# Kernel tuning notes

Measured on AMD Instinct MI355X. Metric: run time of the kernel, lower is better.

Reference implementation:

```python
import jax, jax.numpy as jnp
import numpy as np
from jax import lax

LEAKY_ALPHA = 0.3  # Keras LeakyReLU default


def _conv2d_same(psi, w, b):
    # psi: [B,H,W,Cin], w: [kh,kw,Cin,Cout], b: [Cout]
    y = lax.conv_general_dilated(
        psi, w, window_strides=(1, 1), padding='SAME',
        dimension_numbers=('NHWC', 'HWIO', 'NHWC'))
    y = y + b
    return jnp.where(y > 0, y, LEAKY_ALPHA * y)


def setup_inputs() -> dict:
    key = jax.random.key(0)
    ks = jax.random.split(key, 4)
    B, H, W, BANDS, C = 2, 128, 128, 32, 64
    CPSI = 64
    x = jax.random.normal(ks[0], (B, H, W, BANDS, C), dtype=jnp.float32)
    psi = jax.random.normal(ks[1], (B, H, W, CPSI), dtype=jnp.float32)
    fan_in = 3 * 3 * CPSI
    scale = (2.0 / fan_in) ** 0.5  # he-like init for conv weights
    gamma_w = jax.random.normal(ks[2], (3, 3, CPSI, C), dtype=jnp.float32) * scale
    beta_w = jax.random.normal(ks[3], (3, 3, CPSI, C), dtype=jnp.float32) * scale
    gamma_b = jnp.zeros((C,), dtype=jnp.float32)
    beta_b = jnp.zeros((C,), dtype=jnp.float32)
    return {"x": x, "psi": psi, "gamma_w": gamma_w, "gamma_b": gamma_b,
            "beta_w": beta_w, "beta_b": beta_b}


def reference(x, psi, gamma_w, gamma_b, beta_w, beta_b):
    # SFT / FiLM: gamma, beta conditioned on psi, broadcast over the band axis.
    gamma = _conv2d_same(psi, gamma_w, gamma_b)  # [B,H,W,C]
    beta = _conv2d_same(psi, beta_w, beta_b)     # [B,H,W,C]
    # Original loops over bands with slice/concat; equivalent to one broadcast.
    return gamma[:, :, :, None, :] * x + beta[:, :, :, None, :]  # [B,H,W,bands,C]
```

## Files before the change

### kernel.cpp

```cpp
#include <hip/hip_runtime.h>


#define LEAKY 0.3f

constexpr int Bc    = 2;
constexpr int Hc    = 128;
constexpr int Wc    = 128;
constexpr int BANDS = 32;
constexpr int C     = 64;
constexpr int CPSI  = 64;
constexpr int COUT2 = 128;
constexpr int NPIX  = Bc * Hc * Wc;

typedef __attribute__((ext_vector_type(8))) short bf16x8;
typedef __attribute__((ext_vector_type(4))) float f32x4;

__device__ __forceinline__ unsigned short f2bf(float v) {
  unsigned int u = __float_as_uint(v);
  u += 0x7fffu + ((u >> 16) & 1u);
  return (unsigned short)(u >> 16);
}
__device__ __forceinline__ float bf2f(unsigned short h) {
  return __uint_as_float(((unsigned int)h) << 16);
}

__global__ __launch_bounds__(256) void split_w(
    const float* __restrict__ gw, const float* __restrict__ bw,
    unsigned short* __restrict__ wt)
{
  int o = blockIdx.x * 256 + threadIdx.x;
  int tap = o >> 14;
  int kp  = (o >> 7) & 127;
  int n   = o & 127;
  int cin = kp & 63;
  const float* src = (n < C) ? gw : bw;
  float v = src[((size_t)tap * 64 + cin) * 64 + (n & 63)];
  unsigned short hi = f2bf(v);
  unsigned short r  = (kp < 64) ? hi : f2bf(v - bf2f(hi));
  wt[((size_t)tap << 14) + (size_t)n * 128 + kp] = r;
}

constexpr int AS_BYTES = 3 * 34 * 136 * 2;
constexpr int BS_BYTES = 128 * 136 * 2;
constexpr int SMEM_BYTES = AS_BYTES + BS_BYTES;

__global__ __launch_bounds__(256) void sft_fused(
    const float* __restrict__ psi,
    const unsigned short* __restrict__ wt,
    const float* __restrict__ gbias, const float* __restrict__ bbias,
    const float* __restrict__ x,
    float* __restrict__ out)
{
  __shared__ __align__(16) char smem[SMEM_BYTES];
  auto As = (unsigned short(*)[34][136])smem;
  auto Bs = (unsigned short(*)[136])(smem + AS_BYTES);
  auto g  = (float(*)[132])smem;

  const int tid = threadIdx.x;
  const int blk = blockIdx.x;
  const int w0  = (blk & 3) * 32;
  const int h   = (blk >> 2) & 127;
  const int b   = blk >> 9;
  const int pix0 = blk * 32;

  for (int c = tid; c < 3 * 34 * 16; c += 256) {
    int ch  = c & 15;
    int col = (c >> 4) % 34;
    int row = (c >> 4) / 34;
    int hh = h + row - 1;
    int ww = w0 + col - 1;
    float4 v = make_float4(0.f, 0.f, 0.f, 0.f);
    if (hh >= 0 && hh < Hc && ww >= 0 && ww < Wc)
      v = *(const float4*)&psi[(((size_t)b * Hc + hh) * Wc + ww) * CPSI + ch * 4];
    ushort4 hi, lo;
    hi.x = f2bf(v.x); lo.x = f2bf(v.x - bf2f(hi.x));
    hi.y = f2bf(v.y); lo.y = f2bf(v.y - bf2f(hi.y));
    hi.z = f2bf(v.z); lo.z = f2bf(v.z - bf2f(hi.z));
    hi.w = f2bf(v.w); lo.w = f2bf(v.w - bf2f(hi.w));
    *(ushort4*)&As[row][col][ch * 4]      = hi;
    *(ushort4*)&As[row][col][64 + ch * 4] = lo;
  }

  const int lane = tid & 63;
  const int wv   = tid >> 6;
  const int nb   = wv * 32;
  const int lrow = lane & 15;
  const int lk8  = (lane >> 4) * 8;

  f32x4 acc[2][2];
#pragma unroll
  for (int i = 0; i < 2; ++i)
#pragma unroll
    for (int j = 0; j < 2; ++j) acc[i][j] = (f32x4){0.f, 0.f, 0.f, 0.f};

  for (int c = tid; c < 128 * 16; c += 256) {
    int ch = c & 15, n = c >> 4;
    *(int4*)&Bs[n][ch * 8] = *(const int4*)&wt[(size_t)n * 128 + ch * 8];
  }
  __syncthreads();

  for (int tap = 0; tap < 9; ++tap) {
    const int r  = tap / 3;
    const int dc = tap % 3;

    int4 wreg[8];
    if (tap < 8) {
      const unsigned short* wsrc = wt + ((size_t)(tap + 1) << 14);
#pragma unroll
      for (int i = 0; i < 8; ++i) {
        int c = tid + 256 * i;
        int ch = c & 15, n = c >> 4;
        wreg[i] = *(const int4*)&wsrc[(size_t)n * 128 + ch * 8];
      }
    }

#pragma unroll
    for (int sb = 0; sb < 3; ++sb) {
      const int ao = (sb == 1) ? 64 : 0;
      const int bo = (sb == 2) ? 64 : 0;
#pragma unroll
      for (int kk = 0; kk < 64; kk += 32) {
        bf16x8 af0 = *(const bf16x8*)&As[r][lrow + dc][ao + kk + lk8];
        bf16x8 af1 = *(const bf16x8*)&As[r][16 + lrow + dc][ao + kk + lk8];
        bf16x8 bf0 = *(const bf16x8*)&Bs[nb + lrow][bo + kk + lk8];
        bf16x8 bf1 = *(const bf16x8*)&Bs[nb + 16 + lrow][bo + kk + lk8];
        acc[0][0] = __builtin_amdgcn_mfma_f32_16x16x32_bf16(af0, bf0, acc[0][0], 0, 0, 0);
        acc[0][1] = __builtin_amdgcn_mfma_f32_16x16x32_bf16(af0, bf1, acc[0][1], 0, 0, 0);
        acc[1][0] = __builtin_amdgcn_mfma_f32_16x16x32_bf16(af1, bf0, acc[1][0], 0, 0, 0);
        acc[1][1] = __builtin_amdgcn_mfma_f32_16x16x32_bf16(af1, bf1, acc[1][1], 0, 0, 0);
      }
    }

    if (tap < 8) {
      __syncthreads();
#pragma unroll
      for (int i = 0; i < 8; ++i) {
        int c = tid + 256 * i;
        int ch = c & 15, n = c >> 4;
        *(int4*)&Bs[n][ch * 8] = wreg[i];
      }
      __syncthreads();
    }
  }

  __syncthreads();
#pragma unroll
  for (int nf = 0; nf < 2; ++nf) {
    const int n = nb + nf * 16 + lrow;
    const float bias = (n < C) ? gbias[n] : bbias[n - C];
#pragma unroll
    for (int mf = 0; mf < 2; ++mf) {
#pragma unroll
      for (int rr = 0; rr < 4; ++rr) {
        int m = mf * 16 + (lane >> 4) * 4 + rr;
        float v = acc[mf][nf][rr] + bias;
        g[m][n] = v > 0.f ? v : LEAKY * v;
      }
    }
  }
  __syncthreads();

  const int c0 = (tid * 4) & 63;
  const size_t pbase = (size_t)pix0 * 2048 + (size_t)tid * 4;
#pragma unroll 4
  for (int p = 0; p < 32; ++p) {
    f32x4 ga = *(const f32x4*)&g[p][c0];
    f32x4 be = *(const f32x4*)&g[p][64 + c0];
    size_t a = pbase + (size_t)p * 2048;
    f32x4 x0 = __builtin_nontemporal_load((const f32x4*)&x[a]);
    f32x4 x1 = __builtin_nontemporal_load((const f32x4*)&x[a + 1024]);
    f32x4 o0, o1;
#pragma unroll
    for (int e = 0; e < 4; ++e) {
      o0[e] = fmaf(ga[e], x0[e], be[e]);
      o1[e] = fmaf(ga[e], x1[e], be[e]);
    }
    __builtin_nontemporal_store(o0, (f32x4*)&out[a]);
    __builtin_nontemporal_store(o1, (f32x4*)&out[a + 1024]);
  }
}

__global__ __launch_bounds__(256) void film_fused_slow(
    const float* __restrict__ psi,
    const float* __restrict__ gw, const float* __restrict__ gbias,
    const float* __restrict__ bw, const float* __restrict__ bbias,
    const float* __restrict__ x,
    float* __restrict__ out)
{
  const int pix = blockIdx.x;
  const int w = pix % Wc;
  const int h = (pix / Wc) % Hc;
  const int b = pix / (Wc * Hc);
  __shared__ float pshal[9 * CPSI];
  __shared__ float g[COUT2];
  const int t = threadIdx.x;

  if (t < 144) {
    int j = t * 4;
    int k = j % CPSI;
    int tap = j / CPSI;
    int r = tap / 3, s = tap % 3;
    int hh = h + r - 1, ww = w + s - 1;
    float4 v = make_float4(0.f, 0.f, 0.f, 0.f);
    if (hh >= 0 && hh < Hc && ww >= 0 && ww < Wc)
      v = *(const float4*)&psi[(((size_t)b * Hc + hh) * Wc + ww) * CPSI + k];
    *(float4*)&pshal[j] = v;
  }
  __syncthreads();

  if (t < COUT2) {
    int c = t & 63;
    const float* W_ = (t < C) ? gw : bw;
    float acc = (t < C) ? gbias[c] : bbias[c];
#pragma unroll 4
    for (int j = 0; j < 576; ++j) acc = fmaf(pshal[j], W_[(size_t)j * 64 + c], acc);
    g[t] = acc > 0.f ? acc : LEAKY * acc;
  }
  __syncthreads();

  const int coff = (t & 7) * 8;
  const size_t base = (size_t)pix * (BANDS * C) + (size_t)t * 8;
  float4 x0 = *(const float4*)&x[base];
  float4 x1 = *(const float4*)&x[base + 4];
  float4 ga0 = *(const float4*)&g[coff];
  float4 ga1 = *(const float4*)&g[coff + 4];
  float4 be0 = *(const float4*)&g[C + coff];
  float4 be1 = *(const float4*)&g[C + coff + 4];
  float4 o0, o1;
  o0.x = fmaf(ga0.x, x0.x, be0.x);
  o0.y = fmaf(ga0.y, x0.y, be0.y);
  o0.z = fmaf(ga0.z, x0.z, be0.z);
  o0.w = fmaf(ga0.w, x0.w, be0.w);
  o1.x = fmaf(ga1.x, x1.x, be1.x);
  o1.y = fmaf(ga1.y, x1.y, be1.y);
  o1.z = fmaf(ga1.z, x1.z, be1.z);
  o1.w = fmaf(ga1.w, x1.w, be1.w);
  *(float4*)&out[base] = o0;
  *(float4*)&out[base + 4] = o1;
}

extern "C" void kernel_launch(void* const* d_in, const int* in_sizes, int n_in,
                              void* d_out, int out_size, void* d_ws, size_t ws_size,
                              hipStream_t stream) {
  const float* x     = (const float*)d_in[0];
  const float* psi   = (const float*)d_in[1];
  const float* gw    = (const float*)d_in[2];
  const float* gbias = (const float*)d_in[3];
  const float* bw    = (const float*)d_in[4];
  const float* bbias = (const float*)d_in[5];
  float* out = (float*)d_out;

  const size_t wsplit_bytes = (size_t)9 * 128 * 128 * 2;

  if (ws_size >= wsplit_bytes) {
    unsigned short* wtp = (unsigned short*)d_ws;
    split_w<<<9 * 128 * 128 / 256, 256, 0, stream>>>(gw, bw, wtp);
    sft_fused<<<NPIX / 32, 256, 0, stream>>>(psi, wtp, gbias, bbias, x, out);
  } else {
    film_fused_slow<<<NPIX, 256, 0, stream>>>(psi, gw, gbias, bw, bbias, x, out);
  }
}
```

Measured before the change: 503.6 us.

## Load MFMA weight fragments directly from global memory instead of LDS staging

Drops the shared-memory weight tile and its per-tap register prefetch plus the two barriers per tap. Each lane now reads its B fragments straight from the global (L2-resident) split weights. This roughly halves LDS use, and the launch bounds now request 4 blocks per CU to raise occupancy. The cost is more global load traffic and latency inside the MFMA loop, with no explicit prefetch to hide it.

After: 464.7 us. 7.7% less time.

```diff
diff --git a/kernel.cpp b/kernel.cpp
--- a/kernel.cpp
+++ b/kernel.cpp
@@ -40,11 +40,9 @@
   wt[((size_t)tap << 14) + (size_t)n * 128 + kp] = r;
 }
 
-constexpr int AS_BYTES = 3 * 34 * 136 * 2;
-constexpr int BS_BYTES = 128 * 136 * 2;
-constexpr int SMEM_BYTES = AS_BYTES + BS_BYTES;
-
-__global__ __launch_bounds__(256) void sft_fused(
+constexpr int SMEM_BYTES = 3 * 34 * 136 * 2;
+
+__global__ __launch_bounds__(256, 4) void sft_fused(
     const float* __restrict__ psi,
     const unsigned short* __restrict__ wt,
     const float* __restrict__ gbias, const float* __restrict__ bbias,
@@ -53,7 +51,6 @@
 {
   __shared__ __align__(16) char smem[SMEM_BYTES];
   auto As = (unsigned short(*)[34][136])smem;
-  auto Bs = (unsigned short(*)[136])(smem + AS_BYTES);
   auto g  = (float(*)[132])smem;
 
   const int tid = threadIdx.x;
@@ -93,53 +90,39 @@
 #pragma unroll
     for (int j = 0; j < 2; ++j) acc[i][j] = (f32x4){0.f, 0.f, 0.f, 0.f};
 
-  for (int c = tid; c < 128 * 16; c += 256) {
-    int ch = c & 15, n = c >> 4;
-    *(int4*)&Bs[n][ch * 8] = *(const int4*)&wt[(size_t)n * 128 + ch * 8];
-  }
-  __syncthreads();
+  __syncthreads();
+
+  const unsigned short* wl0 = wt + (size_t)(nb + lrow) * 128 + lk8;
+  const unsigned short* wl1 = wt + (size_t)(nb + 16 + lrow) * 128 + lk8;
 
   for (int tap = 0; tap < 9; ++tap) {
     const int r  = tap / 3;
     const int dc = tap % 3;
-
-    int4 wreg[8];
-    if (tap < 8) {
-      const unsigned short* wsrc = wt + ((size_t)(tap + 1) << 14);
-#pragma unroll
-      for (int i = 0; i < 8; ++i) {
-        int c = tid + 256 * i;
-        int ch = c & 15, n = c >> 4;
-        wreg[i] = *(const int4*)&wsrc[(size_t)n * 128 + ch * 8];
-      }
-    }
-
-#pragma unroll
-    for (int sb = 0; sb < 3; ++sb) {
-      const int ao = (sb == 1) ? 64 : 0;
-      const int bo = (sb == 2) ? 64 : 0;
-#pragma unroll
-      for (int kk = 0; kk < 64; kk += 32) {
-        bf16x8 af0 = *(const bf16x8*)&As[r][lrow + dc][ao + kk + lk8];
-        bf16x8 af1 = *(const bf16x8*)&As[r][16 + lrow + dc][ao + kk + lk8];
-        bf16x8 bf0 = *(const bf16x8*)&Bs[nb + lrow][bo + kk + lk8];
-        bf16x8 bf1 = *(const bf16x8*)&Bs[nb + 16 + lrow][bo + kk + lk8];
-        acc[0][0] = __builtin_amdgcn_mfma_f32_16x16x32_bf16(af0, bf0, acc[0][0], 0, 0, 0);
-        acc[0][1] = __builtin_amdgcn_mfma_f32_16x16x32_bf16(af0, bf1, acc[0][1], 0, 0, 0);
-        acc[1][0] = __builtin_amdgcn_mfma_f32_16x16x32_bf16(af1, bf0, acc[1][0], 0, 0, 0);
-        acc[1][1] = __builtin_amdgcn_mfma_f32_16x16x32_bf16(af1, bf1, acc[1][1], 0, 0, 0);
-      }
-    }
-
-    if (tap < 8) {
-      __syncthreads();
-#pragma unroll
-      for (int i = 0; i < 8; ++i) {
-        int c = tid + 256 * i;
-        int ch = c & 15, n = c >> 4;
-        *(int4*)&Bs[n][ch * 8] = wreg[i];
-      }
-      __syncthreads();
+    const size_t to = (size_t)tap << 14;
+
+#pragma unroll
+    for (int kk = 0; kk < 64; kk += 32) {
+      bf16x8 ah0 = *(const bf16x8*)&As[r][lrow + dc][kk + lk8];
+      bf16x8 ah1 = *(const bf16x8*)&As[r][16 + lrow + dc][kk + lk8];
+      bf16x8 al0 = *(const bf16x8*)&As[r][lrow + dc][64 + kk + lk8];
+      bf16x8 al1 = *(const bf16x8*)&As[r][16 + lrow + dc][64 + kk + lk8];
+      bf16x8 bh0 = *(const bf16x8*)&wl0[to + kk];
+      bf16x8 bh1 = *(const bf16x8*)&wl1[to + kk];
+      bf16x8 bl0 = *(const bf16x8*)&wl0[to + 64 + kk];
+      bf16x8 bl1 = *(const bf16x8*)&wl1[to + 64 + kk];
+
+      acc[0][0] = __builtin_amdgcn_mfma_f32_16x16x32_bf16(ah0, bh0, acc[0][0], 0, 0, 0);
+      acc[0][1] = __builtin_amdgcn_mfma_f32_16x16x32_bf16(ah0, bh1, acc[0][1], 0, 0, 0);
+      acc[1][0] = __builtin_amdgcn_mfma_f32_16x16x32_bf16(ah1, bh0, acc[1][0], 0, 0, 0);
+      acc[1][1] = __builtin_amdgcn_mfma_f32_16x16x32_bf16(ah1, bh1, acc[1][1], 0, 0, 0);
+      acc[0][0] = __builtin_amdgcn_mfma_f32_16x16x32_bf16(al0, bh0, acc[0][0], 0, 0, 0);
+      acc[0][1] = __builtin_amdgcn_mfma_f32_16x16x32_bf16(al0, bh1, acc[0][1], 0, 0, 0);
+      acc[1][0] = __builtin_amdgcn_mfma_f32_16x16x32_bf16(al1, bh0, acc[1][0], 0, 0, 0);
+      acc[1][1] = __builtin_amdgcn_mfma_f32_16x16x32_bf16(al1, bh1, acc[1][1], 0, 0, 0);
+      acc[0][0] = __builtin_amdgcn_mfma_f32_16x16x32_bf16(ah0, bl0, acc[0][0], 0, 0, 0);
+      acc[0][1] = __builtin_amdgcn_mfma_f32_16x16x32_bf16(ah0, bl1, acc[0][1], 0, 0, 0);
+      acc[1][0] = __builtin_amdgcn_mfma_f32_16x16x32_bf16(ah1, bl0, acc[1][0], 0, 0, 0);
+      acc[1][1] = __builtin_amdgcn_mfma_f32_16x16x32_bf16(ah1, bl1, acc[1][1], 0, 0, 0);
     }
   }
 
```
